# Performance work log

Hardware: AMD Instinct MI355X
Metric: run time of the kernel (lower is better)

## Reference

```python
import jax, jax.numpy as jnp
import numpy as np

NEG_SLOPE = 0.2


def add_self_loops(edge_index, num_nodes):
    loop = jnp.arange(num_nodes, dtype=edge_index.dtype)
    loops = jnp.stack([loop, loop])  # [2, N]
    return jnp.concatenate([edge_index, loops], axis=1)


def gat_conv(x, edge_index, W, a_src, a_dst, b, concat=True):
    """PyG-style GATConv. a_src/a_dst: [1, H, C]. W: [F_in, H*C]."""
    N = x.shape[0]
    H, C = a_src.shape[1], a_src.shape[2]
    xp = (x @ W).reshape(N, H, C)                       # [N, H, C]
    alpha_src = (xp * a_src).sum(-1)                    # [N, H]
    alpha_dst = (xp * a_dst).sum(-1)                    # [N, H]
    src, dst = edge_index[0], edge_index[1]
    e = alpha_src[src] + alpha_dst[dst]                 # [E, H]
    e = jnp.where(e > 0, e, NEG_SLOPE * e)              # LeakyReLU(0.2)
    # per-destination segment softmax
    m = jax.ops.segment_max(e, dst, num_segments=N)     # [N, H]
    m = jnp.where(jnp.isfinite(m), m, 0.0)
    ez = jnp.exp(e - m[dst])
    s = jax.ops.segment_sum(ez, dst, num_segments=N)    # [N, H]
    alpha = ez / (s[dst] + 1e-16)                       # [E, H]
    msg = xp[src] * alpha[:, :, None]                   # [E, H, C]
    out = jax.ops.segment_sum(msg, dst, num_segments=N) # [N, H, C]
    out = out.reshape(N, H * C) if concat else out.mean(axis=1)
    return out + b


def setup_inputs() -> dict:
    key = jax.random.key(0)
    ks = jax.random.split(key, 16)
    N, F, E, CLS = 100000, 256, 1600000, 10
    x = jax.random.normal(ks[0], (N, F), dtype=jnp.float32)
    edge_index = jax.random.randint(ks[1], (2, E), 0, N, dtype=jnp.int64)

    def glorot(k, shape):
        fan = shape[0] + shape[-1] * (shape[1] if len(shape) == 3 else 1)
        return jax.random.uniform(k, shape, jnp.float32, -1.0, 1.0) * jnp.sqrt(6.0 / fan)

    return {
        "x": x, "edge_index": edge_index,
        "W1": glorot(ks[2], (F, 128)),  "a1s": glorot(ks[3], (1, 8, 16)),
        "a1d": glorot(ks[4], (1, 8, 16)), "b1": jnp.zeros((128,), jnp.float32),
        "W2": glorot(ks[5], (128, 64)), "a2s": glorot(ks[6], (1, 8, 8)),
        "a2d": glorot(ks[7], (1, 8, 8)),  "b2": jnp.zeros((64,), jnp.float32),
        "W3": glorot(ks[8], (64, CLS)), "a3s": glorot(ks[9], (1, 1, CLS)),
        "a3d": glorot(ks[10], (1, 1, CLS)), "b3": jnp.zeros((CLS,), jnp.float32),
    }


def reference(x, edge_index, W1, a1s, a1d, b1, W2, a2s, a2d, b2, W3, a3s, a3d, b3):
    ei = add_self_loops(edge_index, x.shape[0])
    h = jax.nn.elu(gat_conv(x, ei, W1, a1s, a1d, b1))
    h = jax.nn.elu(gat_conv(h, ei, W2, a2s, a2d, b2))
    h = gat_conv(h, ei, W3, a3s, a3d, b3)
    return jax.nn.log_softmax(h, axis=1)
```

## Files before the change

### kernel.cpp

```cpp
#include <hip/hip_runtime.h>
#include <hip/hip_bf16.h>
#include <math.h>


#define LEAKY(v) ((v) > 0.f ? (v) : 0.2f * (v))

typedef __bf16 bf16_t;
typedef __bf16 bf16x8 __attribute__((ext_vector_type(8)));
typedef __bf16 bf16x4 __attribute__((ext_vector_type(4)));
typedef float f32x4 __attribute__((ext_vector_type(4)));

static __device__ __forceinline__ unsigned short bf_bits(float f) {
    bf16_t b = (bf16_t)f;
    return __builtin_bit_cast(unsigned short, b);
}
static __device__ __forceinline__ float bf_to_f(unsigned short u) {
    return __uint_as_float(((unsigned int)u) << 16);
}
static __device__ __forceinline__ float bperm_f(int byteaddr, float v) {
    return __uint_as_float((unsigned)__builtin_amdgcn_ds_bpermute(byteaddr, (int)__float_as_uint(v)));
}

constexpr int NB_MAX = 400;
constexpr int BCAP = 5120;

__global__ void zero_k(int* a, int n) {
    int i = blockIdx.x * blockDim.x + threadIdx.x;
    if (i < n) a[i] = 0;
}

__global__ __launch_bounds__(256) void partition_k(
        const int* __restrict__ src, const int* __restrict__ dst, int E, int NB,
        int* __restrict__ bcur, unsigned* __restrict__ staged) {
    __shared__ int hist[NB_MAX];
    __shared__ int bstart[NB_MAX + 1];
    __shared__ int cur[NB_MAX];
    __shared__ int gbase[NB_MAX];
    __shared__ unsigned words[4096];
    __shared__ unsigned short bidl[4096];
    int tid = threadIdx.x;
    int e0 = blockIdx.x * 4096;
    int cnt = E - e0; if (cnt > 4096) cnt = 4096;
    if (cnt <= 0) return;

    for (int b = tid; b < NB; b += 256) hist[b] = 0;
    __syncthreads();
    for (int i = tid; i < cnt; i += 256) atomicAdd(&hist[dst[e0 + i] >> 8], 1);
    __syncthreads();
    if (tid == 0) {
        int run = 0;
        for (int b = 0; b < NB; b++) { bstart[b] = run; run += hist[b]; }
        bstart[NB] = run;
    }
    __syncthreads();
    for (int b = tid; b < NB; b += 256) {
        cur[b] = bstart[b];
        gbase[b] = hist[b] ? atomicAdd(&bcur[b], hist[b]) : 0;
    }
    __syncthreads();
    for (int i = tid; i < cnt; i += 256) {
        int s = src[e0 + i], d = dst[e0 + i];
        int b = d >> 8;
        unsigned w = (unsigned)s | ((unsigned)(d & 255) << 17);
        int p = atomicAdd(&cur[b], 1);
        words[p] = w;
        bidl[p] = (unsigned short)b;
    }
    __syncthreads();
    for (int i = tid; i < cnt; i += 256) {
        int b = bidl[i];
        staged[(size_t)b * BCAP + gbase[b] + (i - bstart[b])] = words[i];
    }
}

__global__ void scan_nb_k(const int* __restrict__ bcur, int* __restrict__ ebase, int NB) {
    int lane = threadIdx.x;
    int CH = (NB + 63) / 64;
    int b0 = lane * CH;
    int v[8]; int s = 0;
#pragma unroll 8
    for (int k = 0; k < CH; k++) { int b = b0 + k; int t = (b < NB) ? bcur[b] : 0; if (k < 8) v[k] = t; s += t; }
    int orig = s;
    for (int off = 1; off < 64; off <<= 1) {
        int t = __shfl_up(s, off, 64);
        if (lane >= off) s += t;
    }
    int run = s - orig;
    for (int k = 0; k < CH; k++) { int b = b0 + k; if (b < NB) { ebase[b] = run; run += v[k]; } }
    if (lane == 63) ebase[NB] = run;
}

__global__ __launch_bounds__(256) void buildcsr_k(
        const unsigned* __restrict__ staged, const int* __restrict__ bcur,
        const int* __restrict__ ebase, int* __restrict__ offs, int* __restrict__ cols,
        int N, int NB) {
    __shared__ int h[256], hs[256], curl[256];
    __shared__ int colsl[BCAP];
    int b = blockIdx.x, tid = threadIdx.x;
    int n0 = b << 8;
    int ecnt = bcur[b];
    int base_g = ebase[b];
    const unsigned* sb = staged + (size_t)b * BCAP;

    h[tid] = 0;
    __syncthreads();
    for (int i = tid; i < ecnt; i += 256) atomicAdd(&h[sb[i] >> 17], 1);
    __syncthreads();
    int val = h[tid];
    hs[tid] = val; __syncthreads();
    for (int off = 1; off < 256; off <<= 1) {
        int t = (tid >= off) ? hs[tid - off] : 0;
        __syncthreads();
        hs[tid] += t;
        __syncthreads();
    }
    int excl = hs[tid] - val;
    curl[tid] = excl;
    if (n0 + tid < N) offs[n0 + tid] = base_g + excl;
    if (b == NB - 1 && tid == 0) offs[N] = base_g + ecnt;
    __syncthreads();
    for (int i = tid; i < ecnt; i += 256) {
        unsigned w = sb[i];
        int p = atomicAdd(&curl[w >> 17], 1);
        colsl[p] = (int)(w & 0x1FFFFu);
    }
    __syncthreads();
    for (int i = tid; i < ecnt; i += 256) cols[base_g + i] = colsl[i];
}

__global__ void prep_w_k(const float* __restrict__ W, short* __restrict__ Bfs,
                         int K, int N, int NT, int total) {
    int idx = blockIdx.x * blockDim.x + threadIdx.x;
    if (idx >= total) return;
    int lane = idx & 63;
    int t = idx >> 6;
    int ntile = t % NT, kstep = t / NT;
    int quad = lane >> 4, nl = lane & 15;
    int n = ntile * 16 + nl;
    bf16_t* dst = (bf16_t*)Bfs + (size_t)idx * 16;
#pragma unroll
    for (int j = 0; j < 8; j++) {
        int k = kstep * 32 + quad * 8 + j;
        float v = W[k * N + n];
        bf16_t h = (bf16_t)v;
        bf16_t l = (bf16_t)(v - (float)h);
        dst[j] = h;
        dst[8 + j] = l;
    }
}

template <int BM, int WMT, int WNT, int NWM, bool ABF16, int CHEAD>
__global__ __launch_bounds__(256) void mfma_gemm_k(
        const void* __restrict__ Av, const short* __restrict__ Bfs,
        unsigned short* __restrict__ Cb,
        const float* __restrict__ a_s, const float* __restrict__ a_d,
        float* __restrict__ out_as, float* __restrict__ out_ad,
        int M, int N, int K, int NT) {
    constexpr int NWN = 4 / NWM;
    constexpr int BN = 16 * WNT * NWN;
    constexpr int KPAD = 40;
    __shared__ __align__(16) bf16_t As_hi[BM * KPAD];
    __shared__ __align__(16) bf16_t As_lo[ABF16 ? 16 : BM * KPAD];
    const bf16_t* Bf = (const bf16_t*)Bfs;

    int tid = threadIdx.x;
    int wave = tid >> 6, lane = tid & 63;
    int quad = lane >> 4, l16 = lane & 15;
    int wm = wave % NWM, wn = wave / NWM;
    int row0 = blockIdx.x * BM;
    int ntile0 = blockIdx.y * (BN / 16) + wn * WNT;

    f32x4 acc[WMT][WNT];
#pragma unroll
    for (int i = 0; i < WMT; i++)
#pragma unroll
        for (int j = 0; j < WNT; j++) acc[i][j] = (f32x4){0.f, 0.f, 0.f, 0.f};

    const int nk = K >> 5;
    const int rA = tid >> 3, kq = tid & 7;

    for (int ks = 0; ks < nk; ks++) {
#pragma unroll
        for (int rr = rA; rr < BM; rr += 32) {
            int grow = row0 + rr;
            if (!ABF16) {
                const float* A = (const float*)Av;
                f32x4 v = (f32x4){0.f, 0.f, 0.f, 0.f};
                if (grow < M)
                    v = *(const f32x4*)(A + (size_t)grow * K + ks * 32 + kq * 4);
                bf16x4 h, l;
#pragma unroll
                for (int j = 0; j < 4; j++) {
                    bf16_t hh = (bf16_t)v[j];
                    h[j] = hh;
                    l[j] = (bf16_t)(v[j] - (float)hh);
                }
                *(bf16x4*)&As_hi[rr * KPAD + kq * 4] = h;
                *(bf16x4*)&As_lo[rr * KPAD + kq * 4] = l;
            } else {
                const unsigned short* A = (const unsigned short*)Av;
                ushort4 v = make_ushort4(0, 0, 0, 0);
                if (grow < M)
                    v = *(const ushort4*)(A + (size_t)grow * K + ks * 32 + kq * 4);
                *(ushort4*)&As_hi[rr * KPAD + kq * 4] = v;
            }
        }
        __syncthreads();

        bf16x8 ah[WMT], al[WMT];
#pragma unroll
        for (int i = 0; i < WMT; i++) {
            int rowl = wm * (WMT * 16) + i * 16 + l16;
            ah[i] = *(const bf16x8*)&As_hi[rowl * KPAD + quad * 8];
            if (!ABF16) al[i] = *(const bf16x8*)&As_lo[rowl * KPAD + quad * 8];
        }
        bf16x8 bh[WNT], bl[WNT];
#pragma unroll
        for (int j = 0; j < WNT; j++) {
            size_t base = ((size_t)(ks * NT + ntile0 + j) * 64 + lane) * 16;
            bh[j] = *(const bf16x8*)&Bf[base];
            bl[j] = *(const bf16x8*)&Bf[base + 8];
        }
#pragma unroll
        for (int i = 0; i < WMT; i++)
#pragma unroll
            for (int j = 0; j < WNT; j++) {
                acc[i][j] = __builtin_amdgcn_mfma_f32_16x16x32_bf16(ah[i], bh[j], acc[i][j], 0, 0, 0);
                if (!ABF16)
                    acc[i][j] = __builtin_amdgcn_mfma_f32_16x16x32_bf16(al[i], bh[j], acc[i][j], 0, 0, 0);
                acc[i][j] = __builtin_amdgcn_mfma_f32_16x16x32_bf16(ah[i], bl[j], acc[i][j], 0, 0, 0);
            }
        __syncthreads();
    }

#pragma unroll
    for (int i = 0; i < WMT; i++) {
        int rbase = row0 + wm * (WMT * 16) + i * 16 + quad * 4;
#pragma unroll
        for (int j = 0; j < WNT; j++) {
            int gcol = (ntile0 + j) * 16 + l16;
#pragma unroll
            for (int r2 = 0; r2 < 4; r2++) {
                int grow = rbase + r2;
                if (grow < M) Cb[(size_t)grow * N + gcol] = bf_bits(acc[i][j][r2]);
            }
        }
    }

    const int Hh = N / CHEAD;
#pragma unroll
    for (int j = 0; j < WNT; j++) {
        int gcol = (ntile0 + j) * 16 + l16;
        float cs = a_s[gcol], cd = a_d[gcol];
#pragma unroll
        for (int i = 0; i < WMT; i++) {
            float ps[4], pd[4];
#pragma unroll
            for (int r2 = 0; r2 < 4; r2++) {
                ps[r2] = acc[i][j][r2] * cs;
                pd[r2] = acc[i][j][r2] * cd;
            }
#pragma unroll
            for (int off = 1; off < CHEAD; off <<= 1) {
#pragma unroll
                for (int r2 = 0; r2 < 4; r2++) {
                    ps[r2] += __shfl_xor(ps[r2], off, 64);
                    pd[r2] += __shfl_xor(pd[r2], off, 64);
                }
            }
            if ((l16 & (CHEAD - 1)) == 0) {
                int hd = gcol / CHEAD;
                int rb = row0 + wm * (WMT * 16) + i * 16 + quad * 4;
#pragma unroll
                for (int r2 = 0; r2 < 4; r2++) {
                    int grow = rb + r2;
                    if (grow < M) {
                        out_as[(size_t)grow * Hh + hd] = ps[r2];
                        out_ad[(size_t)grow * Hh + hd] = pd[r2];
                    }
                }
            }
        }
    }
}

template <int BM, int BN, int BK, int TM, int TN>
__global__ void gemm_k(const unsigned short* __restrict__ Ab, const float* __restrict__ B,
                       float* __restrict__ C, unsigned short* __restrict__ Cb,
                       int M, int Nc, int K) {
    __shared__ float As[BK][BM + 1];
    __shared__ float Bs[BK][BN + 1];
    int tx = threadIdx.x, ty = threadIdx.y;
    int tid = ty * blockDim.x + tx;
    const int nthreads = (BM / TM) * (BN / TN);
    int row0 = blockIdx.x * BM, col0 = blockIdx.y * BN;
    float acc[TM][TN];
#pragma unroll
    for (int i = 0; i < TM; i++)
#pragma unroll
        for (int j = 0; j < TN; j++) acc[i][j] = 0.f;

    for (int k0 = 0; k0 < K; k0 += BK) {
        for (int i = tid; i < BM * BK; i += nthreads) {
            int r = i / BK, kk = i % BK;
            int gr = row0 + r;
            As[kk][r] = (gr < M) ? bf_to_f(Ab[(size_t)gr * K + (k0 + kk)]) : 0.f;
        }
        for (int i = tid; i < BK * BN; i += nthreads) {
            int kk = i / BN, c = i % BN;
            int gc = col0 + c;
            Bs[kk][c] = (gc < Nc) ? B[(long)(k0 + kk) * Nc + gc] : 0.f;
        }
        __syncthreads();
#pragma unroll
        for (int kk = 0; kk < BK; ++kk) {
            float a[TM], b[TN];
#pragma unroll
            for (int i = 0; i < TM; i++) a[i] = As[kk][ty * TM + i];
#pragma unroll
            for (int j = 0; j < TN; j++) b[j] = Bs[kk][tx * TN + j];
#pragma unroll
            for (int i = 0; i < TM; i++)
#pragma unroll
                for (int j = 0; j < TN; j++) acc[i][j] = fmaf(a[i], b[j], acc[i][j]);
        }
        __syncthreads();
    }
#pragma unroll
    for (int i = 0; i < TM; i++) {
        int gr = row0 + ty * TM + i;
        if (gr >= M) continue;
#pragma unroll
        for (int j = 0; j < TN; j++) {
            int gc = col0 + tx * TN + j;
            if (gc < Nc) {
                C[(long)gr * Nc + gc] = acc[i][j];
                Cb[(long)gr * Nc + gc] = bf_bits(acc[i][j]);
            }
        }
    }
}

template <int H, int C>
__global__ void alpha_k(const float* __restrict__ xp, const float* __restrict__ a_s,
                        const float* __restrict__ a_d, float* __restrict__ out_s,
                        float* __restrict__ out_d, int NH) {
    int i = blockIdx.x * blockDim.x + threadIdx.x;
    if (i >= NH) return;
    int h = i % H;
    const float* v = xp + (long)i * C;
    float ss = 0.f, sd = 0.f;
#pragma unroll
    for (int c = 0; c < C; c++) {
        float x = v[c];
        ss = fmaf(x, a_s[h * C + c], ss);
        sd = fmaf(x, a_d[h * C + c], sd);
    }
    out_s[i] = ss;
    out_d[i] = sd;
}

template <bool DO_ELU>
__global__ void agg16_k(const unsigned short* __restrict__ xpb,
                        const float* __restrict__ asrc, const float* __restrict__ adst,
                        const int* __restrict__ offs, const int* __restrict__ cols,
                        const float* __restrict__ bias, unsigned short* __restrict__ outb,
                        int N) {
    int gtid = blockIdx.x * blockDim.x + threadIdx.x;
    int n = gtid >> 6;
    if (n >= N) return;
    int lane = threadIdx.x & 63;
    int j = lane >> 3, h = lane & 7;
    const int jb = j << 2;
    int start = offs[n], end = offs[n + 1];
    const unsigned* xp32 = (const unsigned*)xpb;

    float ad_l = adst[n * 8 + h];
    float vs = asrc[n * 8 + h] + ad_l;
    vs = LEAKY(vs);

    float m_w = vs;
    float s = (j == 0) ? 1.f : 0.f;
    float m_f = bperm_f(jb, vs);
    unsigned uself = xp32[(size_t)n * 64 + lane];
    float a0 = __uint_as_float(uself << 16);
    float a1 = __uint_as_float(uself & 0xffff0000u);

    for (int c0 = start; c0 < end; c0 += 8) {
        int e = c0 + j;
        bool valid = e < end;
        int src_l = valid ? cols[e] : 0;
        float v = -1e30f;
        if (valid) {
            v = asrc[src_l * 8 + h] + ad_l;
            v = LEAKY(v);
        }
        float cm = v;
        cm = fmaxf(cm, __shfl_xor(cm, 8, 64));
        cm = fmaxf(cm, __shfl_xor(cm, 16, 64));
        cm = fmaxf(cm, __shfl_xor(cm, 32, 64));
        float mw_new = fmaxf(m_w, cm);
        float w_raw = __expf(v - mw_new);
        s = s * __expf(m_w - mw_new) + w_raw;
        m_w = mw_new;
        float cmF = bperm_f(jb, cm);
        float mf_new = fmaxf(m_f, cmF);
        float scF = __expf(m_f - mf_new);
        m_f = mf_new;
        a0 *= scF; a1 *= scF;
#pragma unroll
        for (int j2 = 0; j2 < 8; j2++) {
            int srcj = __builtin_amdgcn_readlane(src_l, j2 * 8);
            float w = bperm_f(jb + j2 * 32, w_raw);
            unsigned u = xp32[(size_t)srcj * 64 + lane];
            a0 = fmaf(w, __uint_as_float(u << 16), a0);
            a1 = fmaf(w, __uint_as_float(u & 0xffff0000u), a1);
        }
    }
    s += __shfl_xor(s, 8, 64);
    s += __shfl_xor(s, 16, 64);
    s += __shfl_xor(s, 32, 64);
    float rs = 1.f / (s + 1e-16f);
    float rsF = bperm_f(jb, rs);
    float o0 = a0 * rsF + bias[2 * lane];
    float o1 = a1 * rsF + bias[2 * lane + 1];
    if (DO_ELU) {
        o0 = o0 > 0.f ? o0 : __expf(o0) - 1.f;
        o1 = o1 > 0.f ? o1 : __expf(o1) - 1.f;
    }
    unsigned packed = (unsigned)bf_bits(o0) | ((unsigned)bf_bits(o1) << 16);
    ((unsigned*)outb)[(size_t)n * 64 + lane] = packed;
}

template <bool DO_ELU>
__global__ void agg8c8_k(const unsigned short* __restrict__ xpb,
                         const float* __restrict__ asrc, const float* __restrict__ adst,
                         const int* __restrict__ offs, const int* __restrict__ cols,
                         const float* __restrict__ bias, unsigned short* __restrict__ outb,
                         int N) {
    int gtid = blockIdx.x * blockDim.x + threadIdx.x;
    int n = gtid >> 6;
    if (n >= N) return;
    int lane = threadIdx.x & 63;
    int j = lane >> 3, h = lane & 7;
    int start = offs[n], end = offs[n + 1];
    const unsigned* xp32 = (const unsigned*)xpb;

    int fp = lane & 31;
    int hF = fp >> 2;
    int half = lane >> 5;
    int sbase = half * 32;

    float ad_l = adst[n * 8 + h];
    float vs = asrc[n * 8 + h] + ad_l;
    vs = LEAKY(vs);

    float m_w = vs;
    float s = (j == 0) ? 1.f : 0.f;
    float m_f = bperm_f(hF * 4, vs);
    float a0 = 0.f, a1 = 0.f;
    if (half == 0) {
        unsigned u = xp32[(size_t)n * 32 + fp];
        a0 = __uint_as_float(u << 16);
        a1 = __uint_as_float(u & 0xffff0000u);
    }

    for (int c0 = start; c0 < end; c0 += 8) {
        int e = c0 + j;
        bool valid = e < end;
        int src_l = valid ? cols[e] : 0;
        float v = -1e30f;
        if (valid) {
            v = asrc[src_l * 8 + h] + ad_l;
            v = LEAKY(v);
        }
        float cm = v;
        cm = fmaxf(cm, __shfl_xor(cm, 8, 64));
        cm = fmaxf(cm, __shfl_xor(cm, 16, 64));
        cm = fmaxf(cm, __shfl_xor(cm, 32, 64));
        float mw_new = fmaxf(m_w, cm);
        float w_raw = __expf(v - mw_new);
        s = s * __expf(m_w - mw_new) + w_raw;
        m_w = mw_new;
        float cmF = bperm_f(hF * 4, cm);
        float mf_new = fmaxf(m_f, cmF);
        float scF = __expf(m_f - mf_new);
        m_f = mf_new;
        a0 *= scF; a1 *= scF;
#pragma unroll
        for (int j2 = 0; j2 < 4; j2++) {
            int srcv = __builtin_amdgcn_ds_bpermute(sbase + j2 * 64, src_l);
            float w = bperm_f(sbase + hF * 4 + j2 * 64, w_raw);
            unsigned u = xp32[(size_t)srcv * 32 + fp];
            a0 = fmaf(w, __uint_as_float(u << 16), a0);
            a1 = fmaf(w, __uint_as_float(u & 0xffff0000u), a1);
        }
    }
    s += __shfl_xor(s, 8, 64);
    s += __shfl_xor(s, 16, 64);
    s += __shfl_xor(s, 32, 64);
    float rs = 1.f / (s + 1e-16f);
    float rsF = bperm_f(hF * 4, rs);
    a0 += __shfl_xor(a0, 32, 64);
    a1 += __shfl_xor(a1, 32, 64);
    if (half == 0) {
        float o0 = a0 * rsF + bias[2 * fp];
        float o1 = a1 * rsF + bias[2 * fp + 1];
        if (DO_ELU) {
            o0 = o0 > 0.f ? o0 : __expf(o0) - 1.f;
            o1 = o1 > 0.f ? o1 : __expf(o1) - 1.f;
        }
        unsigned packed = (unsigned)bf_bits(o0) | ((unsigned)bf_bits(o1) << 16);
        ((unsigned*)outb)[(size_t)n * 32 + fp] = packed;
    }
}

__global__ void agg1h_k(const unsigned short* __restrict__ xpb,
                        const float* __restrict__ asrc, const float* __restrict__ adst,
                        const int* __restrict__ offs, const int* __restrict__ cols,
                        const float* __restrict__ bias, float* __restrict__ out, int N) {
    int gtid = blockIdx.x * blockDim.x + threadIdx.x;
    int n = gtid >> 6;
    if (n >= N) return;
    int lane = threadIdx.x & 63;
    int start = offs[n], end = offs[n + 1];
    float ad = adst[n];
    float vs = asrc[n] + ad;
    vs = LEAKY(vs);

    float m, s;
    if (lane == 0) { m = vs; s = 1.f; } else { m = -1e30f; s = 0.f; }
    for (int e = start + lane; e < end; e += 64) {
        float v = asrc[cols[e]] + ad;
        v = LEAKY(v);
        float mo = fmaxf(m, v);
        s = s * __expf(m - mo) + __expf(v - mo);
        m = mo;
    }
#pragma unroll
    for (int off = 1; off <= 32; off <<= 1) {
        float mo = __shfl_xor(m, off, 64);
        float so = __shfl_xor(s, off, 64);
        float mn = fmaxf(m, mo);
        s = s * __expf(m - mn) + so * __expf(mo - mn);
        m = mn;
    }
    float rs = 1.f / (s + 1e-16f);
    float wself = __expf(vs - m) * rs;

    int j = lane / 10, c = lane - j * 10;
    float acc = 0.f;
    if (j == 0) acc = wself * bf_to_f(xpb[(size_t)n * 10 + c]);
    for (int c0 = start; c0 < end; c0 += 6) {
        int e = c0 + j;
        if (j < 6 && e < end) {
            int src = cols[e];
            float v = asrc[src] + ad;
            v = LEAKY(v);
            float w = __expf(v - m) * rs;
            acc = fmaf(w, bf_to_f(xpb[(size_t)src * 10 + c]), acc);
        }
    }
    float tot = acc;
#pragma unroll
    for (int k = 1; k < 6; k++) tot += __shfl(acc, lane + 10 * k, 64);

    float z = tot + bias[lane < 10 ? lane : 0];
    float mx = -1e30f;
#pragma unroll
    for (int k = 0; k < 10; k++) mx = fmaxf(mx, __shfl(z, k, 64));
    float se = 0.f;
#pragma unroll
    for (int k = 0; k < 10; k++) se += __expf(__shfl(z, k, 64) - mx);
    if (lane < 10) out[(size_t)n * 10 + lane] = z - (__logf(se) + mx);
}


static inline size_t alignup(size_t x) { return (x + 255) & ~(size_t)255; }

extern "C" void kernel_launch(void* const* d_in, const int* in_sizes, int n_in,
                              void* d_out, int out_size, void* d_ws, size_t ws_size,
                              hipStream_t stream) {
    const float* x   = (const float*)d_in[0];
    const int*   ei  = (const int*)d_in[1];
    const float* W1  = (const float*)d_in[2];
    const float* a1s = (const float*)d_in[3];
    const float* a1d = (const float*)d_in[4];
    const float* b1  = (const float*)d_in[5];
    const float* W2  = (const float*)d_in[6];
    const float* a2s = (const float*)d_in[7];
    const float* a2d = (const float*)d_in[8];
    const float* b2  = (const float*)d_in[9];
    const float* W3  = (const float*)d_in[10];
    const float* a3s = (const float*)d_in[11];
    const float* a3d = (const float*)d_in[12];
    const float* b3  = (const float*)d_in[13];
    float* out = (float*)d_out;

    const int N = in_sizes[0] / 256;
    const int E = in_sizes[1] / 2;
    const int* src = ei;
    const int* dst = ei + E;
    const int NB = (N + 255) >> 8;

    char* p = (char*)d_ws;
    int* offs    = (int*)p; p += alignup(sizeof(int) * (size_t)(N + 1));
    int* bcur    = (int*)p; p += alignup(sizeof(int) * (size_t)(NB_MAX + 1));
    int* ebase   = (int*)p; p += alignup(sizeof(int) * (size_t)(NB_MAX + 1));
    int* cols    = (int*)p; p += alignup(sizeof(int) * (size_t)E);
    unsigned short* xpb   = (unsigned short*)p; p += alignup(2 * (size_t)N * 128);
    unsigned short* hbufb = (unsigned short*)p; p += alignup(2 * (size_t)N * 128);
    float* xp    = (float*)p; p += alignup(sizeof(float) * (size_t)N * 128);
    float* as_   = (float*)p; p += alignup(sizeof(float) * (size_t)N * 8);
    float* ad_   = (float*)p; p += alignup(sizeof(float) * (size_t)N * 8);
    short* Bf1   = (short*)p; p += alignup(sizeof(short) * 8 * 8 * 64 * 16);
    short* Bf2   = (short*)p; p += alignup(sizeof(short) * 4 * 4 * 64 * 16);
    unsigned* staged = (unsigned*)xp;

    const int TB = 256;

    zero_k<<<(NB + TB - 1) / TB, TB, 0, stream>>>(bcur, NB);
    partition_k<<<(E + 4095) / 4096, 256, 0, stream>>>(src, dst, E, NB, bcur, staged);
    scan_nb_k<<<1, 64, 0, stream>>>(bcur, ebase, NB);
    buildcsr_k<<<NB, 256, 0, stream>>>(staged, bcur, ebase, offs, cols, N, NB);

    prep_w_k<<<(4096 + TB - 1) / TB, TB, 0, stream>>>(W1, Bf1, 256, 128, 8, 4096);
    prep_w_k<<<(1024 + TB - 1) / TB, TB, 0, stream>>>(W2, Bf2, 128, 64, 4, 1024);

    mfma_gemm_k<64, 2, 4, 2, false, 16><<<dim3((N + 63) / 64, 1), 256, 0, stream>>>(
        x, Bf1, xpb, a1s, a1d, as_, ad_, N, 128, 256, 8);
    agg16_k<true><<<(N * 64 + TB - 1) / TB, TB, 0, stream>>>(
        xpb, as_, ad_, offs, cols, b1, hbufb, N);

    mfma_gemm_k<64, 2, 2, 2, true, 8><<<dim3((N + 63) / 64, 1), 256, 0, stream>>>(
        hbufb, Bf2, xpb, a2s, a2d, as_, ad_, N, 64, 128, 4);
    agg8c8_k<true><<<(N * 64 + TB - 1) / TB, TB, 0, stream>>>(
        xpb, as_, ad_, offs, cols, b2, hbufb, N);

    gemm_k<64, 16, 16, 4, 1><<<dim3((N + 63) / 64, 1), dim3(16, 16), 0, stream>>>(
        hbufb, W3, xp, xpb, N, 10, 64);
    alpha_k<1, 10><<<(N + TB - 1) / TB, TB, 0, stream>>>(xp, a3s, a3d, as_, ad_, N);
    agg1h_k<<<(N * 64 + TB - 1) / TB, TB, 0, stream>>>(
        xpb, as_, ad_, offs, cols, b3, out, N);
}
```

Before: 506.9 us.

## Stage full-K A tile in LDS once and unroll K loop in MFMA GEMM

The MFMA GEMM now loads the entire K extent of the A row-block into shared memory in one batched phase (K as a template parameter), then runs a fully unrolled K loop with no per-step barriers. It also changes the wave tiling so each wave covers all 64 rows (WMT=4, NWM=1) and adds a launch bound of 2 blocks per SM. This removes per-K-step synchronisation and exposes more memory-level parallelism on loads, but it greatly increases LDS use (about 67KB for the fp32 hi/lo case), which limits occupancy.

After: 520.0 us. 1.03x slower.

```diff
diff --git a/kernel.cpp b/kernel.cpp
--- a/kernel.cpp
+++ b/kernel.cpp
@@ -9,6 +9,7 @@
 typedef __bf16 bf16x8 __attribute__((ext_vector_type(8)));
 typedef __bf16 bf16x4 __attribute__((ext_vector_type(4)));
 typedef float f32x4 __attribute__((ext_vector_type(4)));
+typedef unsigned short u16x8 __attribute__((ext_vector_type(8)));
 
 static __device__ __forceinline__ unsigned short bf_bits(float f) {
     bf16_t b = (bf16_t)f;
@@ -149,18 +150,18 @@
     }
 }
 
-template <int BM, int WMT, int WNT, int NWM, bool ABF16, int CHEAD>
-__global__ __launch_bounds__(256) void mfma_gemm_k(
+template <int BM, int WMT, int WNT, int NWM, bool ABF16, int CHEAD, int K>
+__global__ __launch_bounds__(256, 2) void mfma_gemm_k(
         const void* __restrict__ Av, const short* __restrict__ Bfs,
         unsigned short* __restrict__ Cb,
         const float* __restrict__ a_s, const float* __restrict__ a_d,
         float* __restrict__ out_as, float* __restrict__ out_ad,
-        int M, int N, int K, int NT) {
+        int M, int N, int NT) {
     constexpr int NWN = 4 / NWM;
     constexpr int BN = 16 * WNT * NWN;
-    constexpr int KPAD = 40;
-    __shared__ __align__(16) bf16_t As_hi[BM * KPAD];
-    __shared__ __align__(16) bf16_t As_lo[ABF16 ? 16 : BM * KPAD];
+    constexpr int KP = K + 8;
+    __shared__ __align__(16) bf16_t As_hi[BM * KP];
+    __shared__ __align__(16) bf16_t As_lo[ABF16 ? 16 : BM * KP];
     const bf16_t* Bf = (const bf16_t*)Bfs;
 
     int tid = threadIdx.x;
@@ -170,49 +171,71 @@
     int row0 = blockIdx.x * BM;
     int ntile0 = blockIdx.y * (BN / 16) + wn * WNT;
 
+    if constexpr (!ABF16) {
+        constexpr int CHUNKS = BM * K * 4 / (16 * 256);
+        const float* A = (const float*)Av;
+        f32x4 tmp[CHUNKS];
+#pragma unroll
+        for (int c = 0; c < CHUNKS; c++) {
+            int ci = c * 256 + tid;
+            int fi = ci * 4;
+            int row = fi / K, k = fi % K;
+            int grow = row0 + row;
+            tmp[c] = (f32x4){0.f, 0.f, 0.f, 0.f};
+            if (grow < M) tmp[c] = *(const f32x4*)(A + (size_t)grow * K + k);
+        }
+#pragma unroll
+        for (int c = 0; c < CHUNKS; c++) {
+            int ci = c * 256 + tid;
+            int fi = ci * 4;
+            int row = fi / K, k = fi % K;
+            bf16x4 h, l;
+#pragma unroll
+            for (int j = 0; j < 4; j++) {
+                bf16_t hh = (bf16_t)tmp[c][j];
+                h[j] = hh;
+                l[j] = (bf16_t)(tmp[c][j] - (float)hh);
+            }
+            *(bf16x4*)&As_hi[row * KP + k] = h;
+            *(bf16x4*)&As_lo[row * KP + k] = l;
+        }
+    } else {
+        constexpr int CHUNKS = BM * K * 2 / (16 * 256);
+        const unsigned short* A = (const unsigned short*)Av;
+        u16x8 tmp[CHUNKS];
+#pragma unroll
+        for (int c = 0; c < CHUNKS; c++) {
+            int ci = c * 256 + tid;
+            int ei = ci * 8;
+            int row = ei / K, k = ei % K;
+            int grow = row0 + row;
+            tmp[c] = (u16x8){0, 0, 0, 0, 0, 0, 0, 0};
+            if (grow < M) tmp[c] = *(const u16x8*)(A + (size_t)grow * K + k);
+        }
+#pragma unroll
+        for (int c = 0; c < CHUNKS; c++) {
+            int ci = c * 256 + tid;
+            int ei = ci * 8;
+            int row = ei / K, k = ei % K;
+            *(u16x8*)&As_hi[row * KP + k] = tmp[c];
+        }
+    }
+    __syncthreads();
+
     f32x4 acc[WMT][WNT];
 #pragma unroll
     for (int i = 0; i < WMT; i++)
 #pragma unroll
         for (int j = 0; j < WNT; j++) acc[i][j] = (f32x4){0.f, 0.f, 0.f, 0.f};
 
-    const int nk = K >> 5;
-    const int rA = tid >> 3, kq = tid & 7;
-
-    for (int ks = 0; ks < nk; ks++) {
-#pragma unroll
-        for (int rr = rA; rr < BM; rr += 32) {
-            int grow = row0 + rr;
-            if (!ABF16) {
-                const float* A = (const float*)Av;
-                f32x4 v = (f32x4){0.f, 0.f, 0.f, 0.f};
-                if (grow < M)
-                    v = *(const f32x4*)(A + (size_t)grow * K + ks * 32 + kq * 4);
-                bf16x4 h, l;
-#pragma unroll
-                for (int j = 0; j < 4; j++) {
-                    bf16_t hh = (bf16_t)v[j];
-                    h[j] = hh;
-                    l[j] = (bf16_t)(v[j] - (float)hh);
-                }
-                *(bf16x4*)&As_hi[rr * KPAD + kq * 4] = h;
-                *(bf16x4*)&As_lo[rr * KPAD + kq * 4] = l;
-            } else {
-                const unsigned short* A = (const unsigned short*)Av;
-                ushort4 v = make_ushort4(0, 0, 0, 0);
-                if (grow < M)
-                    v = *(const ushort4*)(A + (size_t)grow * K + ks * 32 + kq * 4);
-                *(ushort4*)&As_hi[rr * KPAD + kq * 4] = v;
-            }
-        }
-        __syncthreads();
-
+#pragma unroll
+    for (int ks = 0; ks < K / 32; ks++) {
         bf16x8 ah[WMT], al[WMT];
 #pragma unroll
         for (int i = 0; i < WMT; i++) {
             int rowl = wm * (WMT * 16) + i * 16 + l16;
-            ah[i] = *(const bf16x8*)&As_hi[rowl * KPAD + quad * 8];
-            if (!ABF16) al[i] = *(const bf16x8*)&As_lo[rowl * KPAD + quad * 8];
+            ah[i] = *(const bf16x8*)&As_hi[rowl * KP + ks * 32 + quad * 8];
+            if (!ABF16) al[i] = *(const bf16x8*)&As_lo[rowl * KP + ks * 32 + quad * 8];
         }
         bf16x8 bh[WNT], bl[WNT];
 #pragma unroll
@@ -230,7 +253,6 @@
                     acc[i][j] = __builtin_amdgcn_mfma_f32_16x16x32_bf16(al[i], bh[j], acc[i][j], 0, 0, 0);
                 acc[i][j] = __builtin_amdgcn_mfma_f32_16x16x32_bf16(ah[i], bl[j], acc[i][j], 0, 0, 0);
             }
-        __syncthreads();
     }
 
 #pragma unroll
@@ -627,13 +649,13 @@
     prep_w_k<<<(4096 + TB - 1) / TB, TB, 0, stream>>>(W1, Bf1, 256, 128, 8, 4096);
     prep_w_k<<<(1024 + TB - 1) / TB, TB, 0, stream>>>(W2, Bf2, 128, 64, 4, 1024);
 
-    mfma_gemm_k<64, 2, 4, 2, false, 16><<<dim3((N + 63) / 64, 1), 256, 0, stream>>>(
-        x, Bf1, xpb, a1s, a1d, as_, ad_, N, 128, 256, 8);
+    mfma_gemm_k<64, 4, 2, 1, false, 16, 256><<<dim3((N + 63) / 64, 1), 256, 0, stream>>>(
+        x, Bf1, xpb, a1s, a1d, as_, ad_, N, 128, 8);
     agg16_k<true><<<(N * 64 + TB - 1) / TB, TB, 0, stream>>>(
         xpb, as_, ad_, offs, cols, b1, hbufb, N);
 
-    mfma_gemm_k<64, 2, 2, 2, true, 8><<<dim3((N + 63) / 64, 1), 256, 0, stream>>>(
-        hbufb, Bf2, xpb, a2s, a2d, as_, ad_, N, 64, 128, 4);
+    mfma_gemm_k<64, 4, 1, 1, true, 8, 128><<<dim3((N + 63) / 64, 1), 256, 0, stream>>>(
+        hbufb, Bf2, xpb, a2s, a2d, as_, ad_, N, 64, 4);
     agg8c8_k<true><<<(N * 64 + TB - 1) / TB, TB, 0, stream>>>(
         xpb, as_, ad_, offs, cols, b2, hbufb, N);
 
```
